# Performance work log

Hardware: AMD Instinct MI355X
Metric: run time of the kernel (lower is better)

The kernel has to match this reference:

```python
import jax, jax.numpy as jnp
import numpy as np

N = 50000
LN_EPS = 1e-5
NEG_SLOPE = 0.2


def layer_norm(x, w, b):
    mu = jnp.mean(x, axis=-1, keepdims=True)
    var = jnp.mean((x - mu) ** 2, axis=-1, keepdims=True)
    return (x - mu) * jax.lax.rsqrt(var + LN_EPS) * w + b


def gat_conv(x, src, dst, W, a_src, a_dst, bias, concat):
    # W: [in, H*D]; a_src/a_dst: [H, D]
    H, D = a_src.shape
    h = (x @ W).reshape(-1, H, D)                      # [N, H, D]
    s = jnp.einsum('nhd,hd->nh', h, a_src)             # alpha contribution of source
    t = jnp.einsum('nhd,hd->nh', h, a_dst)             # alpha contribution of target
    e = jax.nn.leaky_relu(s[src] + t[dst], NEG_SLOPE)  # [E, H] edge logits
    m = jax.ops.segment_max(e, dst, num_segments=N)    # segment softmax over incoming edges
    p = jnp.exp(e - m[dst])
    z = jax.ops.segment_sum(p, dst, num_segments=N)
    alpha = p / (z[dst] + 1e-16)                       # [E, H]
    out = jax.ops.segment_sum(alpha[:, :, None] * h[src], dst, num_segments=N)  # [N, H, D]
    out = out.reshape(N, H * D) if concat else out.mean(axis=1)
    return out + bias


def setup_inputs() -> dict:
    key = jax.random.key(0)
    ks = jax.random.split(key, 16)
    IN, HID, OUT, H1, H2 = 256, 32, 40, 6, 3
    E = 800000
    g = lambda k, shp, fan: jax.random.normal(k, shp, jnp.float32) * (1.0 / np.sqrt(fan))
    inp = {
        'x': jax.random.normal(ks[0], (N, IN), jnp.float32),
        'edge_index': jax.random.randint(ks[1], (2, E), 0, N, jnp.int32),
        'W1': g(ks[2], (IN, H1 * HID), IN), 'a1s': g(ks[3], (H1, HID), HID), 'a1d': g(ks[4], (H1, HID), HID),
        'b1': jnp.zeros((H1 * HID,), jnp.float32),
        'ln1w': jnp.ones((H1 * HID,), jnp.float32), 'ln1b': jnp.zeros((H1 * HID,), jnp.float32),
        'W2': g(ks[5], (H1 * HID, H2 * HID), H1 * HID), 'a2s': g(ks[6], (H2, HID), HID), 'a2d': g(ks[7], (H2, HID), HID),
        'b2': jnp.zeros((H2 * HID,), jnp.float32),
        'ln2w': jnp.ones((H2 * HID,), jnp.float32), 'ln2b': jnp.zeros((H2 * HID,), jnp.float32),
        'W3': g(ks[8], (H2 * HID, 1 * OUT), H2 * HID), 'a3s': g(ks[9], (1, OUT), OUT), 'a3d': g(ks[10], (1, OUT), OUT),
        'b3': jnp.zeros((OUT,), jnp.float32),
        'ln3w': jnp.ones((OUT,), jnp.float32), 'ln3b': jnp.zeros((OUT,), jnp.float32),
    }
    return inp


def reference(x, edge_index, W1, a1s, a1d, b1, ln1w, ln1b,
              W2, a2s, a2d, b2, ln2w, ln2b,
              W3, a3s, a3d, b3, ln3w, ln3b):
    # add self-loops (PyG GATConv default); eval mode -> dropouts are identity
    loop = jnp.arange(N, dtype=edge_index.dtype)
    src = jnp.concatenate([edge_index[0], loop])
    dst = jnp.concatenate([edge_index[1], loop])

    h = gat_conv(x, src, dst, W1, a1s, a1d, b1, concat=True)
    h = jax.nn.elu(layer_norm(h, ln1w, ln1b))
    h = gat_conv(h, src, dst, W2, a2s, a2d, b2, concat=True)
    h = jax.nn.elu(layer_norm(h, ln2w, ln2b))
    h = gat_conv(h, src, dst, W3, a3s, a3d, b3, concat=False)
    h = layer_norm(h, ln3w, ln3b)
    return jax.nn.log_softmax(h, axis=1)
```

## Files before the change

### kernel.cpp

```cpp
#include <hip/hip_runtime.h>
#include <hip/hip_bf16.h>
#include <cstdint>

#define NNODES 50000
#define NEDGES 800000
#define ETOT   (NEDGES + NNODES)
#define LN_EPS 1e-5f
#define NEG_SLOPE 0.2f
#define ELLW   64

typedef __attribute__((ext_vector_type(8))) short s16x8;
typedef __attribute__((ext_vector_type(4))) float f32x4;

__device__ __forceinline__ float bf2f(unsigned short u) {
    return __uint_as_float(((unsigned int)u) << 16);
}
__device__ __forceinline__ unsigned short f2bf(float f) {
    unsigned int u = __float_as_uint(f);
    u += 0x7FFFu + ((u >> 16) & 1u);
    return (unsigned short)(u >> 16);
}
__device__ __forceinline__ float plo32(unsigned u) { return __uint_as_float(u << 16); }
__device__ __forceinline__ float phi32(unsigned u) { return __uint_as_float(u & 0xffff0000u); }


#define W1SZ (192 * 256)
#define W2SZ (96 * 192)
#define W3SZ (48 * 96)

__global__ __launch_bounds__(256) void prep_kernel(const float* __restrict__ W1, const float* __restrict__ W2,
                                                   const float* __restrict__ W3, unsigned short* __restrict__ wt1,
                                                   unsigned short* __restrict__ wt2, unsigned short* __restrict__ wt3,
                                                   int* __restrict__ counts, unsigned short* __restrict__ ell) {
    int i = blockIdx.x * 256 + threadIdx.x;
    if (i < NNODES) {
        counts[i] = 1;
        ell[(size_t)i * ELLW] = (unsigned short)i;
    }
    if (i < W1SZ) {
        int c = i >> 8, k = i & 255;
        int n = c >> 4, r = c & 15;
        wt1[((n * 32 + (k >> 3)) * 16 + r) * 8 + (k & 7)] = f2bf(W1[k * 192 + c]);
    } else if (i < W1SZ + W2SZ) {
        int j = i - W1SZ;
        int c = j / 192, k = j - c * 192;
        int n = c >> 4, r = c & 15;
        wt2[((n * 24 + (k >> 3)) * 16 + r) * 8 + (k & 7)] = f2bf(W2[k * 96 + c]);
    } else if (i < W1SZ + W2SZ + W3SZ) {
        int j = i - (W1SZ + W2SZ);
        int c = j / 96, k = j - c * 96;
        int n = c >> 4, r = c & 15;
        wt3[((n * 12 + (k >> 3)) * 16 + r) * 8 + (k & 7)] = (c < 40) ? f2bf(W3[k * 40 + c]) : (unsigned short)0;
    }
}


template<int K, int F, int CS, int FP, int H, int D, int SPAD, int WSPLIT, int NHW, bool ABF, bool FILL, bool SEMB>
__global__ __launch_bounds__(256, 4) void gemmst_kernel(const void* __restrict__ Xv,
                                                        const unsigned short* __restrict__ Wt,
                                                        unsigned short* __restrict__ C,
                                                        const float* __restrict__ asf, const float* __restrict__ adf,
                                                        float* __restrict__ sbuf, float* __restrict__ tbuf,
                                                        int nrows, int gblocks,
                                                        const int* __restrict__ eidx, int* counts,
                                                        unsigned short* __restrict__ ell, int e) {
    if constexpr (FILL) {
        if (blockIdx.x >= (unsigned)gblocks) {
            int i = ((int)blockIdx.x - gblocks) * 256 + (int)threadIdx.x;
            if (i < e) {
                int sv = eidx[i];
                int d  = eidx[e + i];
                int slot = atomicAdd(&counts[d], 1);
                if (slot < ELLW) ell[(size_t)d * ELLW + slot] = (unsigned short)sv;
            }
            return;
        }
    }
    const int bix = (int)blockIdx.x;

    constexpr int NT  = FP / 16;
    constexpr int NTW = NT / WSPLIT;
    constexpr int TPB = 4 / WSPLIT;

    __shared__ float lds_s[TPB][16][H];
    __shared__ float lds_t[TPB][16][H];

    const int w    = threadIdx.x >> 6;
    const int lane = threadIdx.x & 63;
    const int tile = w / WSPLIT;
    const int sub  = w % WSPLIT;
    const int pb   = sub * NTW;
    const int mbase = (bix * TPB + tile) * 16;
    const int r = lane & 15;
    const int q = lane >> 4;

    if constexpr (WSPLIT == 1) {
        if (mbase >= nrows) return;
    }

    f32x4 acc[NTW];
#pragma unroll
    for (int nn = 0; nn < NTW; ++nn) acc[nn] = (f32x4){0.f, 0.f, 0.f, 0.f};

    int arow = mbase + r;
    if (arow >= nrows) arow = nrows - 1;
    if (arow < 0) arow = 0;
    const unsigned short* xb = (const unsigned short*)Xv + (size_t)arow * K;
    const float* xf = (const float*)Xv + (size_t)arow * K;

#pragma unroll 2
    for (int k0 = 0; k0 < K; k0 += 32) {
        const int kk = k0 + q * 8;
        const unsigned kc = (unsigned)(kk >> 3);
        s16x8 a;
        if constexpr (ABF) {
            a = *reinterpret_cast<const s16x8*>(xb + kk);
        } else {
            float4 lo = *reinterpret_cast<const float4*>(xf + kk);
            float4 hi = *reinterpret_cast<const float4*>(xf + kk + 4);
            a[0] = (short)f2bf(lo.x); a[1] = (short)f2bf(lo.y);
            a[2] = (short)f2bf(lo.z); a[3] = (short)f2bf(lo.w);
            a[4] = (short)f2bf(hi.x); a[5] = (short)f2bf(hi.y);
            a[6] = (short)f2bf(hi.z); a[7] = (short)f2bf(hi.w);
        }
#pragma unroll
        for (int nn = 0; nn < NTW; ++nn) {
            const unsigned gn = (unsigned)(pb + nn);
            s16x8 b = *reinterpret_cast<const s16x8*>(Wt + ((gn * (K / 8) + kc) * 16 + (unsigned)r) * 8);
            acc[nn] = __builtin_amdgcn_mfma_f32_16x16x32_bf16(a, b, acc[nn], 0, 0, 0);
        }
    }

#pragma unroll
    for (int nn = 0; nn < NTW; ++nn) {
        int col = (pb + nn) * 16 + r;
        if (col < F) {
#pragma unroll
            for (int i = 0; i < 4; ++i) {
                int row = mbase + q * 4 + i;
                if (row < nrows) C[(size_t)row * CS + col] = f2bf(acc[nn][i]);
            }
        }
    }

    float ps[4][NHW], pt[4][NHW];
#pragma unroll
    for (int i = 0; i < 4; ++i)
#pragma unroll
        for (int lh = 0; lh < NHW; ++lh) { ps[i][lh] = 0.f; pt[i][lh] = 0.f; }
    const int h_lo = (sub * NTW * 16) / D;
#pragma unroll
    for (int ss = 0; ss < WSPLIT; ++ss) {
        if (ss != sub) continue;
#pragma unroll
        for (int nn = 0; nn < NTW; ++nn) {
            const int gn = ss * NTW + nn;
            const int col = gn * 16 + r;
            const int lh = (gn * 16) / D - (ss * NTW * 16) / D;
            float av = (col < F) ? asf[col] : 0.f;
            float dv = (col < F) ? adf[col] : 0.f;
#pragma unroll
            for (int i = 0; i < 4; ++i) {
                ps[i][lh] = fmaf(acc[nn][i], av, ps[i][lh]);
                pt[i][lh] = fmaf(acc[nn][i], dv, pt[i][lh]);
            }
        }
    }
#pragma unroll
    for (int off = 1; off <= 8; off <<= 1) {
#pragma unroll
        for (int i = 0; i < 4; ++i)
#pragma unroll
            for (int lh = 0; lh < NHW; ++lh) {
                ps[i][lh] += __shfl_xor(ps[i][lh], off);
                pt[i][lh] += __shfl_xor(pt[i][lh], off);
            }
    }

    if constexpr (WSPLIT == 1) {
#pragma unroll
        for (int lh = 0; lh < NHW; ++lh) {
            const int gh = lh;
            if (gh < H && r == gh) {
#pragma unroll
                for (int i = 0; i < 4; ++i) {
                    int row = mbase + q * 4 + i;
                    if (row < nrows) {
                        if constexpr (SEMB) {
                            reinterpret_cast<float*>(C + (size_t)row * CS + F)[gh] = ps[i][lh];
                        } else {
                            sbuf[row * SPAD + gh] = ps[i][lh];
                        }
                        tbuf[row * H + gh] = pt[i][lh];
                    }
                }
            }
        }
    } else {
        constexpr int NE = TPB * 16 * H;
        if ((int)threadIdx.x < NE) {
            int idx = threadIdx.x;
            int t2 = idx / (16 * H), rem = idx % (16 * H);
            lds_s[t2][rem / H][rem % H] = 0.f;
            lds_t[t2][rem / H][rem % H] = 0.f;
        }
        __syncthreads();
#pragma unroll
        for (int lh = 0; lh < NHW; ++lh) {
            const int gh = h_lo + lh;
            if (gh < H && r == gh) {
#pragma unroll
                for (int i = 0; i < 4; ++i) {
                    atomicAdd(&lds_s[tile][q * 4 + i][gh], ps[i][lh]);
                    atomicAdd(&lds_t[tile][q * 4 + i][gh], pt[i][lh]);
                }
            }
        }
        __syncthreads();
        if ((int)threadIdx.x < NE) {
            int idx = threadIdx.x;
            int t2 = idx / (16 * H), rem = idx % (16 * H);
            int rw = rem / H, hh = rem % H;
            int row = bix * TPB * 16 + t2 * 16 + rw;
            if (row < nrows) {
                if constexpr (SEMB) {
                    reinterpret_cast<float*>(C + (size_t)row * CS + F)[hh] = lds_s[t2][rw][hh];
                } else {
                    sbuf[row * SPAD + hh] = lds_s[t2][rw][hh];
                }
                tbuf[row * H + hh] = lds_t[t2][rw][hh];
            }
        }
    }
}


template<int H, int D, int FS, int CPL, int SPAD, int SOFF, int MODE, typename OutT>
__global__ __launch_bounds__(256) void agg10_kernel(const unsigned short* __restrict__ feat,
                                                    const float* __restrict__ sb, const float* __restrict__ tb,
                                                    const int* __restrict__ counts, const unsigned short* __restrict__ ell,
                                                    const float* __restrict__ bias, const float* __restrict__ lnw,
                                                    const float* __restrict__ lnb, OutT* __restrict__ out, int n) {
    constexpr int F = H * D;
    constexpr int NL = F / CPL;
    int wid = (blockIdx.x * blockDim.x + threadIdx.x) >> 6;
    int lane = threadIdx.x & 63;
    if (wid >= n) return;
    const int node = wid;
    const unsigned short* __restrict__ ellp = ell + (size_t)node * ELLW;
    int cnt = counts[node];
    if (cnt > ELLW) cnt = ELLW;
    const bool act = lane < NL;
    const unsigned ch0 = (unsigned)(lane < NL ? lane : 0) * CPL;
    const int h = (int)(ch0 / D);
    const float th = tb[node * H + h];

    float z = 0.f;
    float acc[CPL];
#pragma unroll
    for (int c = 0; c < CPL; ++c) acc[c] = 0.f;

    auto pval = [&](float sv) -> float {
        float e = sv + th;
        e = fmaxf(e, NEG_SLOPE * e);
        return __expf(e);
    };
    auto sval = [&](unsigned b, unsigned i) -> float {
        if constexpr (SOFF > 0) {
            return *reinterpret_cast<const float*>(feat + b + SOFF + 2 * h);
        } else {
            (void)b;
            return sb[i * SPAD + h];
        }
    };
    auto fmae = [&](float p, const unsigned short* fp) {
        if constexpr (CPL == 4) {
            uint2 w = *reinterpret_cast<const uint2*>(fp);
            acc[0] = fmaf(p, plo32(w.x), acc[0]);
            acc[1] = fmaf(p, phi32(w.x), acc[1]);
            acc[2] = fmaf(p, plo32(w.y), acc[2]);
            acc[3] = fmaf(p, phi32(w.y), acc[3]);
        } else if constexpr (CPL == 2) {
            unsigned w = *reinterpret_cast<const unsigned*>(fp);
            acc[0] = fmaf(p, plo32(w), acc[0]);
            acc[1] = fmaf(p, phi32(w), acc[1]);
        } else {
            acc[0] = fmaf(p, bf2f(*fp), acc[0]);
        }
    };

    int j = 0;
    for (; j + 7 < cnt; j += 8) {
        uint4 iv = *reinterpret_cast<const uint4*>(ellp + j);
        unsigned i0 = iv.x & 0xffffu, i1 = iv.x >> 16;
        unsigned i2 = iv.y & 0xffffu, i3 = iv.y >> 16;
        unsigned i4 = iv.z & 0xffffu, i5 = iv.z >> 16;
        unsigned i6 = iv.w & 0xffffu, i7 = iv.w >> 16;
        unsigned b0 = i0 * FS, b1 = i1 * FS, b2 = i2 * FS, b3 = i3 * FS;
        unsigned b4 = i4 * FS, b5 = i5 * FS, b6 = i6 * FS, b7 = i7 * FS;
        if (act) {
            float s0 = sval(b0, i0);
            float s1 = sval(b1, i1);
            float s2 = sval(b2, i2);
            float s3 = sval(b3, i3);
            float s4 = sval(b4, i4);
            float s5 = sval(b5, i5);
            float s6 = sval(b6, i6);
            float s7 = sval(b7, i7);
            if constexpr (CPL == 4) {
                uint2 w0 = *reinterpret_cast<const uint2*>(feat + b0 + ch0);
                uint2 w1 = *reinterpret_cast<const uint2*>(feat + b1 + ch0);
                uint2 w2 = *reinterpret_cast<const uint2*>(feat + b2 + ch0);
                uint2 w3 = *reinterpret_cast<const uint2*>(feat + b3 + ch0);
                uint2 w4 = *reinterpret_cast<const uint2*>(feat + b4 + ch0);
                uint2 w5 = *reinterpret_cast<const uint2*>(feat + b5 + ch0);
                uint2 w6 = *reinterpret_cast<const uint2*>(feat + b6 + ch0);
                uint2 w7 = *reinterpret_cast<const uint2*>(feat + b7 + ch0);
                float p0 = pval(s0), p1 = pval(s1), p2 = pval(s2), p3 = pval(s3);
                float p4 = pval(s4), p5 = pval(s5), p6 = pval(s6), p7 = pval(s7);
                z += ((p0 + p1) + (p2 + p3)) + ((p4 + p5) + (p6 + p7));
                acc[0] = fmaf(p0, plo32(w0.x), acc[0]); acc[1] = fmaf(p0, phi32(w0.x), acc[1]);
                acc[2] = fmaf(p0, plo32(w0.y), acc[2]); acc[3] = fmaf(p0, phi32(w0.y), acc[3]);
                acc[0] = fmaf(p1, plo32(w1.x), acc[0]); acc[1] = fmaf(p1, phi32(w1.x), acc[1]);
                acc[2] = fmaf(p1, plo32(w1.y), acc[2]); acc[3] = fmaf(p1, phi32(w1.y), acc[3]);
                acc[0] = fmaf(p2, plo32(w2.x), acc[0]); acc[1] = fmaf(p2, phi32(w2.x), acc[1]);
                acc[2] = fmaf(p2, plo32(w2.y), acc[2]); acc[3] = fmaf(p2, phi32(w2.y), acc[3]);
                acc[0] = fmaf(p3, plo32(w3.x), acc[0]); acc[1] = fmaf(p3, phi32(w3.x), acc[1]);
                acc[2] = fmaf(p3, plo32(w3.y), acc[2]); acc[3] = fmaf(p3, phi32(w3.y), acc[3]);
                acc[0] = fmaf(p4, plo32(w4.x), acc[0]); acc[1] = fmaf(p4, phi32(w4.x), acc[1]);
                acc[2] = fmaf(p4, plo32(w4.y), acc[2]); acc[3] = fmaf(p4, phi32(w4.y), acc[3]);
                acc[0] = fmaf(p5, plo32(w5.x), acc[0]); acc[1] = fmaf(p5, phi32(w5.x), acc[1]);
                acc[2] = fmaf(p5, plo32(w5.y), acc[2]); acc[3] = fmaf(p5, phi32(w5.y), acc[3]);
                acc[0] = fmaf(p6, plo32(w6.x), acc[0]); acc[1] = fmaf(p6, phi32(w6.x), acc[1]);
                acc[2] = fmaf(p6, plo32(w6.y), acc[2]); acc[3] = fmaf(p6, phi32(w6.y), acc[3]);
                acc[0] = fmaf(p7, plo32(w7.x), acc[0]); acc[1] = fmaf(p7, phi32(w7.x), acc[1]);
                acc[2] = fmaf(p7, plo32(w7.y), acc[2]); acc[3] = fmaf(p7, phi32(w7.y), acc[3]);
            } else if constexpr (CPL == 2) {
                unsigned w0 = *reinterpret_cast<const unsigned*>(feat + b0 + ch0);
                unsigned w1 = *reinterpret_cast<const unsigned*>(feat + b1 + ch0);
                unsigned w2 = *reinterpret_cast<const unsigned*>(feat + b2 + ch0);
                unsigned w3 = *reinterpret_cast<const unsigned*>(feat + b3 + ch0);
                unsigned w4 = *reinterpret_cast<const unsigned*>(feat + b4 + ch0);
                unsigned w5 = *reinterpret_cast<const unsigned*>(feat + b5 + ch0);
                unsigned w6 = *reinterpret_cast<const unsigned*>(feat + b6 + ch0);
                unsigned w7 = *reinterpret_cast<const unsigned*>(feat + b7 + ch0);
                float p0 = pval(s0), p1 = pval(s1), p2 = pval(s2), p3 = pval(s3);
                float p4 = pval(s4), p5 = pval(s5), p6 = pval(s6), p7 = pval(s7);
                z += ((p0 + p1) + (p2 + p3)) + ((p4 + p5) + (p6 + p7));
                acc[0] = fmaf(p0, plo32(w0), acc[0]); acc[1] = fmaf(p0, phi32(w0), acc[1]);
                acc[0] = fmaf(p1, plo32(w1), acc[0]); acc[1] = fmaf(p1, phi32(w1), acc[1]);
                acc[0] = fmaf(p2, plo32(w2), acc[0]); acc[1] = fmaf(p2, phi32(w2), acc[1]);
                acc[0] = fmaf(p3, plo32(w3), acc[0]); acc[1] = fmaf(p3, phi32(w3), acc[1]);
                acc[0] = fmaf(p4, plo32(w4), acc[0]); acc[1] = fmaf(p4, phi32(w4), acc[1]);
                acc[0] = fmaf(p5, plo32(w5), acc[0]); acc[1] = fmaf(p5, phi32(w5), acc[1]);
                acc[0] = fmaf(p6, plo32(w6), acc[0]); acc[1] = fmaf(p6, phi32(w6), acc[1]);
                acc[0] = fmaf(p7, plo32(w7), acc[0]); acc[1] = fmaf(p7, phi32(w7), acc[1]);
            } else {
                unsigned short w0 = feat[b0 + ch0], w1 = feat[b1 + ch0], w2 = feat[b2 + ch0], w3 = feat[b3 + ch0];
                unsigned short w4 = feat[b4 + ch0], w5 = feat[b5 + ch0], w6 = feat[b6 + ch0], w7 = feat[b7 + ch0];
                float p0 = pval(s0), p1 = pval(s1), p2 = pval(s2), p3 = pval(s3);
                float p4 = pval(s4), p5 = pval(s5), p6 = pval(s6), p7 = pval(s7);
                z += ((p0 + p1) + (p2 + p3)) + ((p4 + p5) + (p6 + p7));
                acc[0] = fmaf(p0, bf2f(w0), acc[0]);
                acc[0] = fmaf(p1, bf2f(w1), acc[0]);
                acc[0] = fmaf(p2, bf2f(w2), acc[0]);
                acc[0] = fmaf(p3, bf2f(w3), acc[0]);
                acc[0] = fmaf(p4, bf2f(w4), acc[0]);
                acc[0] = fmaf(p5, bf2f(w5), acc[0]);
                acc[0] = fmaf(p6, bf2f(w6), acc[0]);
                acc[0] = fmaf(p7, bf2f(w7), acc[0]);
            }
        }
    }
    for (; j + 3 < cnt; j += 4) {
        uint2 iv = *reinterpret_cast<const uint2*>(ellp + j);
        unsigned i0 = iv.x & 0xffffu, i1 = iv.x >> 16;
        unsigned i2 = iv.y & 0xffffu, i3 = iv.y >> 16;
        unsigned b0 = i0 * FS, b1 = i1 * FS, b2 = i2 * FS, b3 = i3 * FS;
        if (act) {
            float p0 = pval(sval(b0, i0));
            float p1 = pval(sval(b1, i1));
            float p2 = pval(sval(b2, i2));
            float p3 = pval(sval(b3, i3));
            z += (p0 + p1) + (p2 + p3);
            fmae(p0, feat + b0 + ch0);
            fmae(p1, feat + b1 + ch0);
            fmae(p2, feat + b2 + ch0);
            fmae(p3, feat + b3 + ch0);
        }
    }
    for (; j < cnt; ++j) {
        unsigned sn = ellp[j];
        unsigned b = sn * FS;
        if (act) {
            float p = pval(sval(b, sn));
            z += p;
            fmae(p, feat + b + ch0);
        }
    }

    const float zinv = 1.f / (z + 1e-16f);
    float v[CPL];
    float sum = 0.f, sumsq = 0.f;
#pragma unroll
    for (int c = 0; c < CPL; ++c) v[c] = 0.f;
    if (act) {
#pragma unroll
        for (int c = 0; c < CPL; ++c) {
            v[c] = fmaf(acc[c], zinv, bias[ch0 + c]);
            sum += v[c];
            sumsq += v[c] * v[c];
        }
    }
#pragma unroll
    for (int off = 32; off; off >>= 1) {
        sum += __shfl_xor(sum, off);
        sumsq += __shfl_xor(sumsq, off);
    }
    const float mu = sum / F;
    const float var = sumsq / F - mu * mu;
    const float rstd = rsqrtf(var + LN_EPS);

    if (MODE == 0) {
        if (act) {
            unsigned short yb[CPL];
#pragma unroll
            for (int c = 0; c < CPL; ++c) {
                float y = (v[c] - mu) * rstd * lnw[ch0 + c] + lnb[ch0 + c];
                y = y > 0.f ? y : expm1f(y);
                yb[c] = f2bf(y);
            }
            OutT* op = out + (size_t)node * F + ch0;
            if constexpr (CPL == 4) {
                ushort4 st = {yb[0], yb[1], yb[2], yb[3]};
                *reinterpret_cast<ushort4*>(op) = st;
            } else if constexpr (CPL == 2) {
                ushort2 st = {yb[0], yb[1]};
                *reinterpret_cast<ushort2*>(op) = st;
            } else {
                *op = yb[0];
            }
        }
    } else {
        float y = 0.f, mx = -1e30f;
        if (act) {
            y = (v[0] - mu) * rstd * lnw[ch0] + lnb[ch0];
            mx = y;
        }
#pragma unroll
        for (int off = 32; off; off >>= 1) mx = fmaxf(mx, __shfl_xor(mx, off));
        float se = act ? __expf(y - mx) : 0.f;
#pragma unroll
        for (int off = 32; off; off >>= 1) se += __shfl_xor(se, off);
        float lse = logf(se);
        if (act) ((float*)out)[(size_t)node * F + ch0] = y - mx - lse;
    }
}


static inline size_t align_up(size_t x) { return (x + 255) & ~(size_t)255; }

extern "C" void kernel_launch(void* const* d_in, const int* in_sizes, int n_in,
                              void* d_out, int out_size, void* d_ws, size_t ws_size,
                              hipStream_t stream) {
    const float* x    = (const float*)d_in[0];
    const int*   eidx = (const int*)d_in[1];
    const float* W1   = (const float*)d_in[2];
    const float* a1s  = (const float*)d_in[3];
    const float* a1d  = (const float*)d_in[4];
    const float* b1   = (const float*)d_in[5];
    const float* ln1w = (const float*)d_in[6];
    const float* ln1b = (const float*)d_in[7];
    const float* W2   = (const float*)d_in[8];
    const float* a2s  = (const float*)d_in[9];
    const float* a2d  = (const float*)d_in[10];
    const float* b2   = (const float*)d_in[11];
    const float* ln2w = (const float*)d_in[12];
    const float* ln2b = (const float*)d_in[13];
    const float* W3   = (const float*)d_in[14];
    const float* a3s  = (const float*)d_in[15];
    const float* a3d  = (const float*)d_in[16];
    const float* b3   = (const float*)d_in[17];
    const float* ln3w = (const float*)d_in[18];
    const float* ln3b = (const float*)d_in[19];

    char* w = (char*)d_ws;
    int* counts = (int*)w;  w += align_up((size_t)NNODES * 4);
    unsigned short* ell = (unsigned short*)w;  w += align_up((size_t)NNODES * ELLW * 2);
    unsigned short* bufA = (unsigned short*)w; w += align_up((size_t)NNODES * 192 * 2);
    unsigned short* bufB = (unsigned short*)w; w += align_up((size_t)NNODES * 192 * 2);
    float* sbuf = (float*)w; w += align_up((size_t)NNODES * 8 * 4);
    float* tbuf = (float*)w; w += align_up((size_t)NNODES * 8 * 4);
    unsigned short* wt1 = (unsigned short*)w; w += align_up((size_t)W1SZ * 2);
    unsigned short* wt2 = (unsigned short*)w; w += align_up((size_t)W2SZ * 2);
    unsigned short* wt3 = (unsigned short*)w; w += align_up((size_t)W3SZ * 2);

    const int BS = 256;
    const int PREP_N = W1SZ + W2SZ + W3SZ;
    prep_kernel<<<(PREP_N + BS - 1) / BS, BS, 0, stream>>>(W1, W2, W3, wt1, wt2, wt3, counts, ell);

    const int G1 = NNODES / 16;
    const int G2 = (NNODES + 31) / 32;
    const int G3 = (NNODES + 63) / 64;
    const int FILL_NB  = (NEDGES + BS - 1) / BS;
    const int GRID_AGG = (NNODES + 3) / 4;

    gemmst_kernel<256, 192, 192, 192, 6, 32, 8, 4, 2, false, true, false>
        <<<G1 + FILL_NB, BS, 0, stream>>>(x, wt1, bufA, a1s, a1d, sbuf, tbuf, NNODES,
                                          G1, eidx, counts, ell, NEDGES);
    agg10_kernel<6, 32, 192, 4, 8, 0, 0, unsigned short><<<GRID_AGG, BS, 0, stream>>>(bufA, sbuf, tbuf, counts, ell, b1, ln1w, ln1b, bufB, NNODES);

    gemmst_kernel<192, 96, 128, 96, 3, 32, 4, 2, 2, true, false, true>
        <<<G2, BS, 0, stream>>>(bufB, wt2, bufA, a2s, a2d, sbuf, tbuf, NNODES,
                                G2, nullptr, nullptr, nullptr, 0);
    agg10_kernel<3, 32, 128, 2, 4, 96, 0, unsigned short><<<GRID_AGG, BS, 0, stream>>>(bufA, sbuf, tbuf, counts, ell, b2, ln2w, ln2b, bufB, NNODES);

    gemmst_kernel<96, 40, 64, 48, 1, 40, 1, 1, 1, true, false, true>
        <<<G3, BS, 0, stream>>>(bufB, wt3, bufA, a3s, a3d, sbuf, tbuf, NNODES,
                                G3, nullptr, nullptr, nullptr, 0);
    agg10_kernel<1, 40, 64, 1, 1, 40, 1, float><<<GRID_AGG, BS, 0, stream>>>(bufA, sbuf, tbuf, counts, ell, b3, ln3w, ln3b, (float*)d_out, NNODES);
}
```

Before: 260.6 us.

## Fuse GAT aggregation with next layer's projection GEMM and attention scores

Layers 1 and 2 each get a new kernel that aggregates 16 nodes per block (4 per wave), writes the normalized ELU rows to shared memory, and immediately runs the next layer's MFMA projection and attention dot products. This removes two separate GEMM launches and the global write and re-read of the intermediate activations. In exchange each block does serial per-node gathers before its GEMM, and per-block parallelism changes. Occupancy could also drop because of the added shared memory and registers.

```diff
diff --git a/kernel.cpp b/kernel.cpp
--- a/kernel.cpp
+++ b/kernel.cpp
@@ -55,7 +55,7 @@
 }
 
 
-template<int K, int F, int CS, int FP, int H, int D, int SPAD, int WSPLIT, int NHW, bool ABF, bool FILL, bool SEMB>
+template<int K, int F, int CS, int FP, int H, int D, int SPAD, int WSPLIT, int NHW, bool ABF, bool FILL>
 __global__ __launch_bounds__(256, 4) void gemmst_kernel(const void* __restrict__ Xv,
                                                         const unsigned short* __restrict__ Wt,
                                                         unsigned short* __restrict__ C,
@@ -94,10 +94,6 @@
     const int r = lane & 15;
     const int q = lane >> 4;
 
-    if constexpr (WSPLIT == 1) {
-        if (mbase >= nrows) return;
-    }
-
     f32x4 acc[NTW];
 #pragma unroll
     for (int nn = 0; nn < NTW; ++nn) acc[nn] = (f32x4){0.f, 0.f, 0.f, 0.f};
@@ -177,86 +173,55 @@
             }
     }
 
-    if constexpr (WSPLIT == 1) {
-#pragma unroll
-        for (int lh = 0; lh < NHW; ++lh) {
-            const int gh = lh;
-            if (gh < H && r == gh) {
-#pragma unroll
-                for (int i = 0; i < 4; ++i) {
-                    int row = mbase + q * 4 + i;
-                    if (row < nrows) {
-                        if constexpr (SEMB) {
-                            reinterpret_cast<float*>(C + (size_t)row * CS + F)[gh] = ps[i][lh];
-                        } else {
-                            sbuf[row * SPAD + gh] = ps[i][lh];
-                        }
-                        tbuf[row * H + gh] = pt[i][lh];
-                    }
-                }
-            }
-        }
-    } else {
-        constexpr int NE = TPB * 16 * H;
-        if ((int)threadIdx.x < NE) {
-            int idx = threadIdx.x;
-            int t2 = idx / (16 * H), rem = idx % (16 * H);
-            lds_s[t2][rem / H][rem % H] = 0.f;
-            lds_t[t2][rem / H][rem % H] = 0.f;
-        }
-        __syncthreads();
-#pragma unroll
-        for (int lh = 0; lh < NHW; ++lh) {
-            const int gh = h_lo + lh;
-            if (gh < H && r == gh) {
-#pragma unroll
-                for (int i = 0; i < 4; ++i) {
-                    atomicAdd(&lds_s[tile][q * 4 + i][gh], ps[i][lh]);
-                    atomicAdd(&lds_t[tile][q * 4 + i][gh], pt[i][lh]);
-                }
-            }
-        }
-        __syncthreads();
-        if ((int)threadIdx.x < NE) {
-            int idx = threadIdx.x;
-            int t2 = idx / (16 * H), rem = idx % (16 * H);
-            int rw = rem / H, hh = rem % H;
-            int row = bix * TPB * 16 + t2 * 16 + rw;
-            if (row < nrows) {
-                if constexpr (SEMB) {
-                    reinterpret_cast<float*>(C + (size_t)row * CS + F)[hh] = lds_s[t2][rw][hh];
-                } else {
-                    sbuf[row * SPAD + hh] = lds_s[t2][rw][hh];
-                }
-                tbuf[row * H + hh] = lds_t[t2][rw][hh];
-            }
-        }
-    }
-}
-
-
-template<int H, int D, int FS, int CPL, int SPAD, int SOFF, int MODE, typename OutT>
-__global__ __launch_bounds__(256) void agg10_kernel(const unsigned short* __restrict__ feat,
-                                                    const float* __restrict__ sb, const float* __restrict__ tb,
-                                                    const int* __restrict__ counts, const unsigned short* __restrict__ ell,
-                                                    const float* __restrict__ bias, const float* __restrict__ lnw,
-                                                    const float* __restrict__ lnb, OutT* __restrict__ out, int n) {
+    constexpr int NE = TPB * 16 * H;
+    if ((int)threadIdx.x < NE) {
+        int idx = threadIdx.x;
+        int t2 = idx / (16 * H), rem = idx % (16 * H);
+        lds_s[t2][rem / H][rem % H] = 0.f;
+        lds_t[t2][rem / H][rem % H] = 0.f;
+    }
+    __syncthreads();
+#pragma unroll
+    for (int lh = 0; lh < NHW; ++lh) {
+        const int gh = h_lo + lh;
+        if (gh < H && r == gh) {
+#pragma unroll
+            for (int i = 0; i < 4; ++i) {
+                atomicAdd(&lds_s[tile][q * 4 + i][gh], ps[i][lh]);
+                atomicAdd(&lds_t[tile][q * 4 + i][gh], pt[i][lh]);
+            }
+        }
+    }
+    __syncthreads();
+    if ((int)threadIdx.x < NE) {
+        int idx = threadIdx.x;
+        int t2 = idx / (16 * H), rem = idx % (16 * H);
+        int rw = rem / H, hh = rem % H;
+        int row = bix * TPB * 16 + t2 * 16 + rw;
+        if (row < nrows) {
+            sbuf[row * SPAD + hh] = lds_s[t2][rw][hh];
+            tbuf[row * H + hh]    = lds_t[t2][rw][hh];
+        }
+    }
+}
+
+
+template<int H, int D, int FS, int CPL, int SPAD, int SOFF>
+__device__ __forceinline__ float gat_gather(const unsigned short* __restrict__ feat,
+                                            const float* __restrict__ sb, const float* __restrict__ tb,
+                                            const int* __restrict__ counts, const unsigned short* __restrict__ ell,
+                                            int node, int lane, float (&acc)[CPL]) {
     constexpr int F = H * D;
     constexpr int NL = F / CPL;
-    int wid = (blockIdx.x * blockDim.x + threadIdx.x) >> 6;
-    int lane = threadIdx.x & 63;
-    if (wid >= n) return;
-    const int node = wid;
     const unsigned short* __restrict__ ellp = ell + (size_t)node * ELLW;
     int cnt = counts[node];
     if (cnt > ELLW) cnt = ELLW;
     const bool act = lane < NL;
-    const unsigned ch0 = (unsigned)(lane < NL ? lane : 0) * CPL;
+    const unsigned ch0 = (unsigned)(act ? lane : 0) * CPL;
     const int h = (int)(ch0 / D);
     const float th = tb[node * H + h];
 
     float z = 0.f;
-    float acc[CPL];
 #pragma unroll
     for (int c = 0; c < CPL; ++c) acc[c] = 0.f;
 
@@ -275,15 +240,15 @@
     };
     auto fmae = [&](float p, const unsigned short* fp) {
         if constexpr (CPL == 4) {
-            uint2 w = *reinterpret_cast<const uint2*>(fp);
-            acc[0] = fmaf(p, plo32(w.x), acc[0]);
-            acc[1] = fmaf(p, phi32(w.x), acc[1]);
-            acc[2] = fmaf(p, plo32(w.y), acc[2]);
-            acc[3] = fmaf(p, phi32(w.y), acc[3]);
+            uint2 wq = *reinterpret_cast<const uint2*>(fp);
+            acc[0] = fmaf(p, plo32(wq.x), acc[0]);
+            acc[1] = fmaf(p, phi32(wq.x), acc[1]);
+            acc[2] = fmaf(p, plo32(wq.y), acc[2]);
+            acc[3] = fmaf(p, phi32(wq.y), acc[3]);
         } else if constexpr (CPL == 2) {
-            unsigned w = *reinterpret_cast<const unsigned*>(fp);
-            acc[0] = fmaf(p, plo32(w), acc[0]);
-            acc[1] = fmaf(p, phi32(w), acc[1]);
+            unsigned wq = *reinterpret_cast<const unsigned*>(fp);
+            acc[0] = fmaf(p, plo32(wq), acc[0]);
+            acc[1] = fmaf(p, phi32(wq), acc[1]);
         } else {
             acc[0] = fmaf(p, bf2f(*fp), acc[0]);
         }
@@ -307,69 +272,17 @@
             float s5 = sval(b5, i5);
             float s6 = sval(b6, i6);
             float s7 = sval(b7, i7);
-            if constexpr (CPL == 4) {
-                uint2 w0 = *reinterpret_cast<const uint2*>(feat + b0 + ch0);
-                uint2 w1 = *reinterpret_cast<const uint2*>(feat + b1 + ch0);
-                uint2 w2 = *reinterpret_cast<const uint2*>(feat + b2 + ch0);
-                uint2 w3 = *reinterpret_cast<const uint2*>(feat + b3 + ch0);
-                uint2 w4 = *reinterpret_cast<const uint2*>(feat + b4 + ch0);
-                uint2 w5 = *reinterpret_cast<const uint2*>(feat + b5 + ch0);
-                uint2 w6 = *reinterpret_cast<const uint2*>(feat + b6 + ch0);
-                uint2 w7 = *reinterpret_cast<const uint2*>(feat + b7 + ch0);
-                float p0 = pval(s0), p1 = pval(s1), p2 = pval(s2), p3 = pval(s3);
-                float p4 = pval(s4), p5 = pval(s5), p6 = pval(s6), p7 = pval(s7);
-                z += ((p0 + p1) + (p2 + p3)) + ((p4 + p5) + (p6 + p7));
-                acc[0] = fmaf(p0, plo32(w0.x), acc[0]); acc[1] = fmaf(p0, phi32(w0.x), acc[1]);
-                acc[2] = fmaf(p0, plo32(w0.y), acc[2]); acc[3] = fmaf(p0, phi32(w0.y), acc[3]);
-                acc[0] = fmaf(p1, plo32(w1.x), acc[0]); acc[1] = fmaf(p1, phi32(w1.x), acc[1]);
-                acc[2] = fmaf(p1, plo32(w1.y), acc[2]); acc[3] = fmaf(p1, phi32(w1.y), acc[3]);
-                acc[0] = fmaf(p2, plo32(w2.x), acc[0]); acc[1] = fmaf(p2, phi32(w2.x), acc[1]);
-                acc[2] = fmaf(p2, plo32(w2.y), acc[2]); acc[3] = fmaf(p2, phi32(w2.y), acc[3]);
-                acc[0] = fmaf(p3, plo32(w3.x), acc[0]); acc[1] = fmaf(p3, phi32(w3.x), acc[1]);
-                acc[2] = fmaf(p3, plo32(w3.y), acc[2]); acc[3] = fmaf(p3, phi32(w3.y), acc[3]);
-                acc[0] = fmaf(p4, plo32(w4.x), acc[0]); acc[1] = fmaf(p4, phi32(w4.x), acc[1]);
-                acc[2] = fmaf(p4, plo32(w4.y), acc[2]); acc[3] = fmaf(p4, phi32(w4.y), acc[3]);
-                acc[0] = fmaf(p5, plo32(w5.x), acc[0]); acc[1] = fmaf(p5, phi32(w5.x), acc[1]);
-                acc[2] = fmaf(p5, plo32(w5.y), acc[2]); acc[3] = fmaf(p5, phi32(w5.y), acc[3]);
-                acc[0] = fmaf(p6, plo32(w6.x), acc[0]); acc[1] = fmaf(p6, phi32(w6.x), acc[1]);
-                acc[2] = fmaf(p6, plo32(w6.y), acc[2]); acc[3] = fmaf(p6, phi32(w6.y), acc[3]);
-                acc[0] = fmaf(p7, plo32(w7.x), acc[0]); acc[1] = fmaf(p7, phi32(w7.x), acc[1]);
-                acc[2] = fmaf(p7, plo32(w7.y), acc[2]); acc[3] = fmaf(p7, phi32(w7.y), acc[3]);
-            } else if constexpr (CPL == 2) {
-                unsigned w0 = *reinterpret_cast<const unsigned*>(feat + b0 + ch0);
-                unsigned w1 = *reinterpret_cast<const unsigned*>(feat + b1 + ch0);
-                unsigned w2 = *reinterpret_cast<const unsigned*>(feat + b2 + ch0);
-                unsigned w3 = *reinterpret_cast<const unsigned*>(feat + b3 + ch0);
-                unsigned w4 = *reinterpret_cast<const unsigned*>(feat + b4 + ch0);
-                unsigned w5 = *reinterpret_cast<const unsigned*>(feat + b5 + ch0);
-                unsigned w6 = *reinterpret_cast<const unsigned*>(feat + b6 + ch0);
-                unsigned w7 = *reinterpret_cast<const unsigned*>(feat + b7 + ch0);
-                float p0 = pval(s0), p1 = pval(s1), p2 = pval(s2), p3 = pval(s3);
-                float p4 = pval(s4), p5 = pval(s5), p6 = pval(s6), p7 = pval(s7);
-                z += ((p0 + p1) + (p2 + p3)) + ((p4 + p5) + (p6 + p7));
-                acc[0] = fmaf(p0, plo32(w0), acc[0]); acc[1] = fmaf(p0, phi32(w0), acc[1]);
-                acc[0] = fmaf(p1, plo32(w1), acc[0]); acc[1] = fmaf(p1, phi32(w1), acc[1]);
-                acc[0] = fmaf(p2, plo32(w2), acc[0]); acc[1] = fmaf(p2, phi32(w2), acc[1]);
-                acc[0] = fmaf(p3, plo32(w3), acc[0]); acc[1] = fmaf(p3, phi32(w3), acc[1]);
-                acc[0] = fmaf(p4, plo32(w4), acc[0]); acc[1] = fmaf(p4, phi32(w4), acc[1]);
-                acc[0] = fmaf(p5, plo32(w5), acc[0]); acc[1] = fmaf(p5, phi32(w5), acc[1]);
-                acc[0] = fmaf(p6, plo32(w6), acc[0]); acc[1] = fmaf(p6, phi32(w6), acc[1]);
-                acc[0] = fmaf(p7, plo32(w7), acc[0]); acc[1] = fmaf(p7, phi32(w7), acc[1]);
-            } else {
-                unsigned short w0 = feat[b0 + ch0], w1 = feat[b1 + ch0], w2 = feat[b2 + ch0], w3 = feat[b3 + ch0];
-                unsigned short w4 = feat[b4 + ch0], w5 = feat[b5 + ch0], w6 = feat[b6 + ch0], w7 = feat[b7 + ch0];
-                float p0 = pval(s0), p1 = pval(s1), p2 = pval(s2), p3 = pval(s3);
-                float p4 = pval(s4), p5 = pval(s5), p6 = pval(s6), p7 = pval(s7);
-                z += ((p0 + p1) + (p2 + p3)) + ((p4 + p5) + (p6 + p7));
-                acc[0] = fmaf(p0, bf2f(w0), acc[0]);
-                acc[0] = fmaf(p1, bf2f(w1), acc[0]);
-                acc[0] = fmaf(p2, bf2f(w2), acc[0]);
-                acc[0] = fmaf(p3, bf2f(w3), acc[0]);
-                acc[0] = fmaf(p4, bf2f(w4), acc[0]);
-                acc[0] = fmaf(p5, bf2f(w5), acc[0]);
-                acc[0] = fmaf(p6, bf2f(w6), acc[0]);
-                acc[0] = fmaf(p7, bf2f(w7), acc[0]);
-            }
+            float p0 = pval(s0), p1 = pval(s1), p2 = pval(s2), p3 = pval(s3);
+            float p4 = pval(s4), p5 = pval(s5), p6 = pval(s6), p7 = pval(s7);
+            z += ((p0 + p1) + (p2 + p3)) + ((p4 + p5) + (p6 + p7));
+            fmae(p0, feat + b0 + ch0);
+            fmae(p1, feat + b1 + ch0);
+            fmae(p2, feat + b2 + ch0);
+            fmae(p3, feat + b3 + ch0);
+            fmae(p4, feat + b4 + ch0);
+            fmae(p5, feat + b5 + ch0);
+            fmae(p6, feat + b6 + ch0);
+            fmae(p7, feat + b7 + ch0);
         }
     }
     for (; j + 3 < cnt; j += 4) {
@@ -398,30 +311,70 @@
             fmae(p, feat + b + ch0);
         }
     }
-
-    const float zinv = 1.f / (z + 1e-16f);
-    float v[CPL];
-    float sum = 0.f, sumsq = 0.f;
-#pragma unroll
-    for (int c = 0; c < CPL; ++c) v[c] = 0.f;
-    if (act) {
-#pragma unroll
-        for (int c = 0; c < CPL; ++c) {
-            v[c] = fmaf(acc[c], zinv, bias[ch0 + c]);
-            sum += v[c];
-            sumsq += v[c] * v[c];
-        }
-    }
-#pragma unroll
-    for (int off = 32; off; off >>= 1) {
-        sum += __shfl_xor(sum, off);
-        sumsq += __shfl_xor(sumsq, off);
-    }
-    const float mu = sum / F;
-    const float var = sumsq / F - mu * mu;
-    const float rstd = rsqrtf(var + LN_EPS);
-
-    if (MODE == 0) {
+    return z;
+}
+
+
+template<int H, int D, int FS, int CPL, int SPAD, int SOFF,
+         int F2, int CS2, int FP2, int H2, int D2, int SOFF2>
+__global__ __launch_bounds__(256, 4) void aggmm_kernel(const unsigned short* __restrict__ feat,
+                                                       const float* __restrict__ sb, const float* __restrict__ tbin,
+                                                       const int* __restrict__ counts, const unsigned short* __restrict__ ell,
+                                                       const float* __restrict__ bias, const float* __restrict__ lnw,
+                                                       const float* __restrict__ lnb,
+                                                       const unsigned short* __restrict__ Wt2,
+                                                       const float* __restrict__ asf2, const float* __restrict__ adf2,
+                                                       unsigned short* __restrict__ C2, float* __restrict__ tbout,
+                                                       int n) {
+    constexpr int F   = H * D;
+    constexpr int NL  = F / CPL;
+    constexpr int NT2 = FP2 / 16;
+    constexpr int NP  = (NT2 + 3) / 4;
+
+    __shared__ unsigned short arows[16][200];
+    __shared__ float lds_s[16][H2];
+    __shared__ float lds_t[16][H2];
+
+    const int wv   = threadIdx.x >> 6;
+    const int lane = threadIdx.x & 63;
+    const int r = lane & 15, q = lane >> 4;
+    const int nb = (int)blockIdx.x * 16;
+    (void)n;
+
+    if ((int)threadIdx.x < 16 * H2) {
+        lds_s[threadIdx.x / H2][threadIdx.x % H2] = 0.f;
+        lds_t[threadIdx.x / H2][threadIdx.x % H2] = 0.f;
+    }
+
+    const bool act = lane < NL;
+    const unsigned ch0 = (unsigned)(act ? lane : 0) * CPL;
+
+    for (int u = 0; u < 4; ++u) {
+        const int node = nb + wv * 4 + u;
+        float acc[CPL];
+        float z = gat_gather<H, D, FS, CPL, SPAD, SOFF>(feat, sb, tbin, counts, ell, node, lane, acc);
+
+        const float zinv = 1.f / (z + 1e-16f);
+        float v[CPL];
+        float sum = 0.f, sumsq = 0.f;
+#pragma unroll
+        for (int c = 0; c < CPL; ++c) v[c] = 0.f;
+        if (act) {
+#pragma unroll
+            for (int c = 0; c < CPL; ++c) {
+                v[c] = fmaf(acc[c], zinv, bias[ch0 + c]);
+                sum += v[c];
+                sumsq += v[c] * v[c];
+            }
+        }
+#pragma unroll
+        for (int off = 32; off; off >>= 1) {
+            sum += __shfl_xor(sum, off);
+            sumsq += __shfl_xor(sumsq, off);
+        }
+        const float mu = sum / F;
+        const float var = sumsq / F - mu * mu;
+        const float rstd = rsqrtf(var + LN_EPS);
         if (act) {
             unsigned short yb[CPL];
 #pragma unroll
@@ -430,31 +383,144 @@
                 y = y > 0.f ? y : expm1f(y);
                 yb[c] = f2bf(y);
             }
-            OutT* op = out + (size_t)node * F + ch0;
+            unsigned short* rp = &arows[wv * 4 + u][ch0];
             if constexpr (CPL == 4) {
                 ushort4 st = {yb[0], yb[1], yb[2], yb[3]};
-                *reinterpret_cast<ushort4*>(op) = st;
+                *reinterpret_cast<ushort4*>(rp) = st;
             } else if constexpr (CPL == 2) {
                 ushort2 st = {yb[0], yb[1]};
-                *reinterpret_cast<ushort2*>(op) = st;
+                *reinterpret_cast<ushort2*>(rp) = st;
             } else {
-                *op = yb[0];
-            }
-        }
-    } else {
-        float y = 0.f, mx = -1e30f;
-        if (act) {
-            y = (v[0] - mu) * rstd * lnw[ch0] + lnb[ch0];
-            mx = y;
-        }
-#pragma unroll
-        for (int off = 32; off; off >>= 1) mx = fmaxf(mx, __shfl_xor(mx, off));
-        float se = act ? __expf(y - mx) : 0.f;
-#pragma unroll
-        for (int off = 32; off; off >>= 1) se += __shfl_xor(se, off);
-        float lse = logf(se);
-        if (act) ((float*)out)[(size_t)node * F + ch0] = y - mx - lse;
-    }
+                *rp = yb[0];
+            }
+        }
+    }
+    __syncthreads();
+
+    f32x4 acc2[NP];
+#pragma unroll
+    for (int pi = 0; pi < NP; ++pi) acc2[pi] = (f32x4){0.f, 0.f, 0.f, 0.f};
+
+#pragma unroll 2
+    for (int k0 = 0; k0 < F; k0 += 32) {
+        const int kk = k0 + q * 8;
+        const unsigned kc = (unsigned)(kk >> 3);
+        s16x8 a = *reinterpret_cast<const s16x8*>(&arows[r][kk]);
+#pragma unroll
+        for (int pi = 0; pi < NP; ++pi) {
+            const int gn = wv + 4 * pi;
+            if (gn < NT2) {
+                s16x8 b = *reinterpret_cast<const s16x8*>(Wt2 + (((unsigned)gn * (F / 8) + kc) * 16 + (unsigned)r) * 8);
+                acc2[pi] = __builtin_amdgcn_mfma_f32_16x16x32_bf16(a, b, acc2[pi], 0, 0, 0);
+            }
+        }
+    }
+
+    float ps[4][NP], pt[4][NP];
+#pragma unroll
+    for (int i = 0; i < 4; ++i)
+#pragma unroll
+        for (int pi = 0; pi < NP; ++pi) { ps[i][pi] = 0.f; pt[i][pi] = 0.f; }
+
+#pragma unroll
+    for (int pi = 0; pi < NP; ++pi) {
+        const int gn = wv + 4 * pi;
+        if (gn < NT2) {
+            const int col = gn * 16 + r;
+            const float av = (col < F2) ? asf2[col] : 0.f;
+            const float dv = (col < F2) ? adf2[col] : 0.f;
+            if (col < F2) {
+#pragma unroll
+                for (int i = 0; i < 4; ++i)
+                    C2[(size_t)(nb + q * 4 + i) * CS2 + col] = f2bf(acc2[pi][i]);
+            }
+#pragma unroll
+            for (int i = 0; i < 4; ++i) {
+                ps[i][pi] = acc2[pi][i] * av;
+                pt[i][pi] = acc2[pi][i] * dv;
+            }
+        }
+    }
+#pragma unroll
+    for (int off = 1; off <= 8; off <<= 1) {
+#pragma unroll
+        for (int i = 0; i < 4; ++i)
+#pragma unroll
+            for (int pi = 0; pi < NP; ++pi) {
+                ps[i][pi] += __shfl_xor(ps[i][pi], off);
+                pt[i][pi] += __shfl_xor(pt[i][pi], off);
+            }
+    }
+    if (r == 0) {
+#pragma unroll
+        for (int pi = 0; pi < NP; ++pi) {
+            const int gn = wv + 4 * pi;
+            if (gn < NT2) {
+                const int gh = (gn * 16) / D2;
+#pragma unroll
+                for (int i = 0; i < 4; ++i) {
+                    atomicAdd(&lds_s[q * 4 + i][gh], ps[i][pi]);
+                    atomicAdd(&lds_t[q * 4 + i][gh], pt[i][pi]);
+                }
+            }
+        }
+    }
+    __syncthreads();
+    if ((int)threadIdx.x < 16 * H2) {
+        int ln = threadIdx.x / H2, hh = threadIdx.x % H2;
+        int node = nb + ln;
+        *reinterpret_cast<float*>(C2 + (size_t)node * CS2 + SOFF2 + 2 * hh) = lds_s[ln][hh];
+        tbout[node * H2 + hh] = lds_t[ln][hh];
+    }
+}
+
+
+template<int H, int D, int FS, int CPL, int SPAD, int SOFF>
+__global__ __launch_bounds__(256) void aggfin_kernel(const unsigned short* __restrict__ feat,
+                                                     const float* __restrict__ sb, const float* __restrict__ tb,
+                                                     const int* __restrict__ counts, const unsigned short* __restrict__ ell,
+                                                     const float* __restrict__ bias, const float* __restrict__ lnw,
+                                                     const float* __restrict__ lnb, float* __restrict__ out, int n) {
+    constexpr int F = H * D;
+    constexpr int NL = F / CPL;
+    int wid = (blockIdx.x * blockDim.x + threadIdx.x) >> 6;
+    int lane = threadIdx.x & 63;
+    if (wid >= n) return;
+    const int node = wid;
+    const bool act = lane < NL;
+    const unsigned ch0 = (unsigned)(act ? lane : 0) * CPL;
+
+    float acc[CPL];
+    float z = gat_gather<H, D, FS, CPL, SPAD, SOFF>(feat, sb, tb, counts, ell, node, lane, acc);
+
+    const float zinv = 1.f / (z + 1e-16f);
+    float v = 0.f, sum = 0.f, sumsq = 0.f;
+    if (act) {
+        v = fmaf(acc[0], zinv, bias[ch0]);
+        sum = v;
+        sumsq = v * v;
+    }
+#pragma unroll
+    for (int off = 32; off; off >>= 1) {
+        sum += __shfl_xor(sum, off);
+        sumsq += __shfl_xor(sumsq, off);
+    }
+    const float mu = sum / F;
+    const float var = sumsq / F - mu * mu;
+    const float rstd = rsqrtf(var + LN_EPS);
+
+    float y = 0.f, mx = -1e30f;
+    if (act) {
+        y = (v - mu) * rstd * lnw[ch0] + lnb[ch0];
+        mx = y;
+    }
+#pragma unroll
+    for (int off = 32; off; off >>= 1) mx = fmaxf(mx, __shfl_xor(mx, off));
+    float se = act ? __expf(y - mx) : 0.f;
+#pragma unroll
+    for (int off = 32; off; off >>= 1) se += __shfl_xor(se, off);
+    float lse = logf(se);
+    if (act) out[(size_t)node * F + ch0] = y - mx - lse;
 }
 
 
@@ -488,9 +554,10 @@
     int* counts = (int*)w;  w += align_up((size_t)NNODES * 4);
     unsigned short* ell = (unsigned short*)w;  w += align_up((size_t)NNODES * ELLW * 2);
     unsigned short* bufA = (unsigned short*)w; w += align_up((size_t)NNODES * 192 * 2);
-    unsigned short* bufB = (unsigned short*)w; w += align_up((size_t)NNODES * 192 * 2);
-    float* sbuf = (float*)w; w += align_up((size_t)NNODES * 8 * 4);
-    float* tbuf = (float*)w; w += align_up((size_t)NNODES * 8 * 4);
+    unsigned short* bufB = (unsigned short*)w; w += align_up((size_t)NNODES * 128 * 2);
+    float* sbuf  = (float*)w; w += align_up((size_t)NNODES * 8 * 4);
+    float* tbufA = (float*)w; w += align_up((size_t)NNODES * 6 * 4);
+    float* tbufB = (float*)w; w += align_up((size_t)NNODES * 6 * 4);
     unsigned short* wt1 = (unsigned short*)w; w += align_up((size_t)W1SZ * 2);
     unsigned short* wt2 = (unsigned short*)w; w += align_up((size_t)W2SZ * 2);
     unsigned short* wt3 = (unsigned short*)w; w += align_up((size_t)W3SZ * 2);
@@ -500,23 +567,22 @@
     prep_kernel<<<(PREP_N + BS - 1) / BS, BS, 0, stream>>>(W1, W2, W3, wt1, wt2, wt3, counts, ell);
 
     const int G1 = NNODES / 16;
-    const int G2 = (NNODES + 31) / 32;
-    const int G3 = (NNODES + 63) / 64;
     const int FILL_NB  = (NEDGES + BS - 1) / BS;
+    const int GRID_AMM = NNODES / 16;
     const int GRID_AGG = (NNODES + 3) / 4;
 
-    gemmst_kernel<256, 192, 192, 192, 6, 32, 8, 4, 2, false, true, false>
-        <<<G1 + FILL_NB, BS, 0, stream>>>(x, wt1, bufA, a1s, a1d, sbuf, tbuf, NNODES,
+    gemmst_kernel<256, 192, 192, 192, 6, 32, 8, 4, 2, false, true>
+        <<<G1 + FILL_NB, BS, 0, stream>>>(x, wt1, bufA, a1s, a1d, sbuf, tbufA, NNODES,
                                           G1, eidx, counts, ell, NEDGES);
-    agg10_kernel<6, 32, 192, 4, 8, 0, 0, unsigned short><<<GRID_AGG, BS, 0, stream>>>(bufA, sbuf, tbuf, counts, ell, b1, ln1w, ln1b, bufB, NNODES);
-
-    gemmst_kernel<192, 96, 128, 96, 3, 32, 4, 2, 2, true, false, true>
-        <<<G2, BS, 0, stream>>>(bufB, wt2, bufA, a2s, a2d, sbuf, tbuf, NNODES,
-                                G2, nullptr, nullptr, nullptr, 0);
-    agg10_kernel<3, 32, 128, 2, 4, 96, 0, unsigned short><<<GRID_AGG, BS, 0, stream>>>(bufA, sbuf, tbuf, counts, ell, b2, ln2w, ln2b, bufB, NNODES);
-
-    gemmst_kernel<96, 40, 64, 48, 1, 40, 1, 1, 1, true, false, true>
-        <<<G3, BS, 0, stream>>>(bufB, wt3, bufA, a3s, a3d, sbuf, tbuf, NNODES,
-                                G3, nullptr, nullptr, nullptr, 0);
-    agg10_kernel<1, 40, 64, 1, 1, 40, 1, float><<<GRID_AGG, BS, 0, stream>>>(bufA, sbuf, tbuf, counts, ell, b3, ln3w, ln3b, (float*)d_out, NNODES);
-}
+
+    aggmm_kernel<6, 32, 192, 4, 8, 0,   96, 128, 96, 3, 32, 96>
+        <<<GRID_AMM, BS, 0, stream>>>(bufA, sbuf, tbufA, counts, ell, b1, ln1w, ln1b,
+                                      wt2, a2s, a2d, bufB, tbufB, NNODES);
+
+    aggmm_kernel<3, 32, 128, 2, 4, 96,  40, 64, 48, 1, 40, 40>
+        <<<GRID_AMM, BS, 0, stream>>>(bufB, sbuf, tbufB, counts, ell, b2, ln2w, ln2b,
+                                      wt3, a3s, a3d, bufA, tbufA, NNODES);
+
+    aggfin_kernel<1, 40, 64, 1, 1, 40>
+        <<<GRID_AGG, BS, 0, stream>>>(bufA, sbuf, tbufA, counts, ell, b3, ln3w, ln3b, (float*)d_out, NNODES);
+}
```

After: 268.6 us. 1.03x slower.
